# Kernel tuning notes

Hardware: AMD Instinct MI355X
Metric: run time of the kernel (lower is better)

## Reference

```python
import jax, jax.numpy as jnp
import numpy as np

FEATS = 768
HEAD = 12


def _phi(t):
    # elu feature map + 1 (guarantees positivity)
    return jax.nn.elu(t) + 1.0


def setup_inputs() -> dict:
    key = jax.random.key(0)
    ks = jax.random.split(key, 9)
    f = FEATS
    s = 1.0 / np.sqrt(f)
    x = jax.random.normal(ks[0], (4, 4096, f), dtype=jnp.float32)
    # weights stored as [in, out] so projection is x @ W + b
    Wq = jax.random.normal(ks[1], (f, f), dtype=jnp.float32) * s
    bq = jax.random.normal(ks[2], (f,), dtype=jnp.float32) * 0.01
    Wk = jax.random.normal(ks[3], (f, f), dtype=jnp.float32) * s
    bk = jax.random.normal(ks[4], (f,), dtype=jnp.float32) * 0.01
    Wv = jax.random.normal(ks[5], (f, f), dtype=jnp.float32) * s
    bv = jax.random.normal(ks[6], (f,), dtype=jnp.float32) * 0.01
    Wo = jax.random.normal(ks[7], (f, f), dtype=jnp.float32) * s
    bo = jax.random.normal(ks[8], (f,), dtype=jnp.float32) * 0.01
    return {"x": x, "Wq": Wq, "bq": bq, "Wk": Wk, "bk": bk,
            "Wv": Wv, "bv": bv, "Wo": Wo, "bo": bo}


def reference(x, Wq, bq, Wk, bk, Wv, bv, Wo, bo):
    b, n, f = x.shape
    h = HEAD
    d = f // h
    # project and split heads: [b, h, n, d]
    def heads(t):
        return t.reshape(b, n, h, d).transpose(0, 2, 1, 3)
    q = _phi(heads(x @ Wq + bq))
    k = _phi(heads(x @ Wk + bk))
    v = heads(x @ Wv + bv)
    # kv summary: [b, h, d, d] (sum over sequence)
    kv = jnp.einsum('bhnd,bhne->bhde', k, v)
    # normalizer: z[b,h,l] = 1 / (q[b,h,l,:] . sum_n k[b,h,n,:])  (no eps, as in source)
    ksum = k.sum(axis=2)                      # [b, h, d]
    z = 1.0 / jnp.einsum('bhld,bhd->bhl', q, ksum)  # [b, h, n]
    num = jnp.einsum('bhld,bhde->bhle', q, kv)      # [b, h, n, d]
    normed = num * z[..., None]                     # [b, h, n, d]
    out = normed.transpose(0, 2, 1, 3).reshape(b, n, f)  # [b, n, f]
    return out @ Wo + bo  # dropout p=0.0 -> identity
```

## Files before the change

### kernel.cpp

```cpp
#include <hip/hip_runtime.h>
#include <cstdint>
#include <cstddef>

#define DEVI __device__ __forceinline__

typedef short    shortx8 __attribute__((ext_vector_type(8)));
typedef short    shortx4 __attribute__((ext_vector_type(4)));
typedef short    shortx2 __attribute__((ext_vector_type(2)));
typedef __bf16   bf16x8  __attribute__((ext_vector_type(8)));
typedef float    floatx4 __attribute__((ext_vector_type(4)));

DEVI unsigned short f2b(float f) {
    union { float f; unsigned u; } a; a.f = f;
    unsigned r = a.u + 0x7fffu + ((a.u >> 16) & 1u);
    return (unsigned short)(r >> 16);
}
DEVI float b2f(unsigned short u) {
    union { unsigned u; float f; } a; a.u = ((unsigned)u) << 16;
    return a.f;
}

DEVI floatx4 mfma_bf16(bf16x8 a, bf16x8 b, floatx4 c) {
    return __builtin_amdgcn_mfma_f32_16x16x32_bf16(a, b, c, 0, 0, 0);
}

DEVI void glds16(const ushort* g, ushort* l) {
    __builtin_amdgcn_global_load_lds(
        (const __attribute__((address_space(1))) void*)g,
        (__attribute__((address_space(3))) void*)l, 16, 0, 0);
}

__global__ void k_prep(const float* __restrict__ x, ushort* __restrict__ xb,
                       const float* __restrict__ Wq, const float* __restrict__ Wk,
                       const float* __restrict__ Wv, const float* __restrict__ Wo,
                       ushort* __restrict__ Wt, ushort* __restrict__ Wot,
                       const float* __restrict__ bq, const float* __restrict__ bk,
                       const float* __restrict__ bv, float* __restrict__ bqkv) {
    __shared__ float tile[64][65];
    const int bid = blockIdx.x, t = threadIdx.x;
    if (bid < 6144) {
        size_t i = ((size_t)bid * 256 + t) * 8;
        float4 v0 = *(const float4*)(x + i);
        float4 v1 = *(const float4*)(x + i + 4);
        shortx8 o;
        o[0] = (short)f2b(v0.x); o[1] = (short)f2b(v0.y);
        o[2] = (short)f2b(v0.z); o[3] = (short)f2b(v0.w);
        o[4] = (short)f2b(v1.x); o[5] = (short)f2b(v1.y);
        o[6] = (short)f2b(v1.z); o[7] = (short)f2b(v1.w);
        *(shortx8*)(xb + i) = o;
    } else if (bid < 6720) {
        int pid = bid - 6144;
        int zi = pid / 144, rem = pid % 144;
        const float* W = (zi == 0) ? Wq : (zi == 1) ? Wk : (zi == 2) ? Wv : Wo;
        const int i0 = (rem / 12) * 64, j0 = (rem % 12) * 64;
        const int c = t & 63, r4 = t >> 6;
        for (int rr = r4; rr < 64; rr += 4)
            tile[rr][c] = W[(size_t)(i0 + rr) * 768 + j0 + c];
        __syncthreads();
        ushort* dst = (zi < 3) ? (Wt + (size_t)(zi * 768) * 768) : Wot;
        for (int jj = r4; jj < 64; jj += 4)
            dst[(size_t)(j0 + jj) * 768 + i0 + c] = f2b(tile[c][jj]);
    } else {
        int j = (bid - 6720) * 256 + t;
        if (j < 2304) {
            const float* src = (j < 768) ? bq : (j < 1536) ? bk : bv;
            bqkv[j] = src[j % 768];
        }
    }
}

template <int MODE>
__global__ __launch_bounds__(256, 4) void k_gemm(
    const ushort* __restrict__ A, const ushort* __restrict__ Bt,
    const float* __restrict__ bias, void* __restrict__ Cout, int Ncols) {
    constexpr int K = 768;
    constexpr int GY = (MODE == 0) ? 18 : 6;
    constexpr int NWG = 128 * GY;
    __shared__ ushort As[128 * 64];
    __shared__ ushort Bs[128 * 64];

    const int lin  = blockIdx.y * 128 + blockIdx.x;
    const int wg   = (lin & 7) * (NWG / 8) + (lin >> 3);
    const int band = wg / (8 * GY);
    const int rem  = wg % (8 * GY);
    const int m0 = (band * 8 + (rem & 7)) * 128;
    const int n0 = (rem >> 3) * 128;

    const int tid = threadIdx.x;
    const int w = tid >> 6, lane = tid & 63;

    const int lr = lane >> 3;
    const int lc = ((lane & 7) ^ lr) * 8;
    const ushort* aBase = A  + (size_t)(m0 + w * 32 + lr) * K + lc;
    const ushort* bBase = Bt + (size_t)(n0 + w * 32 + lr) * K + lc;
    ushort* aL = As + (w * 32) * 64;
    ushort* bL = Bs + (w * 32) * 64;

    const int rBase = (w >> 1) * 64;
    const int nBase = (w & 1) * 64;
    const int fr = lane & 15;
    const int q4 = lane >> 4;

    floatx4 acc[4][4] = {};

    for (int k0 = 0; k0 < K; k0 += 64) {
#pragma unroll
        for (int i = 0; i < 4; ++i) glds16(aBase + i * (8 * K) + k0, aL + i * (8 * 64));
#pragma unroll
        for (int i = 0; i < 4; ++i) glds16(bBase + i * (8 * K) + k0, bL + i * (8 * 64));
        __syncthreads();
#pragma unroll
        for (int kc = 0; kc < 2; ++kc) {
            const int off = ((kc * 4 + q4) ^ (fr & 7)) * 8;
            bf16x8 af[4], bf[4];
#pragma unroll
            for (int rt = 0; rt < 4; ++rt)
                af[rt] = *(const bf16x8*)(As + (rBase + rt * 16 + fr) * 64 + off);
#pragma unroll
            for (int nt = 0; nt < 4; ++nt)
                bf[nt] = *(const bf16x8*)(Bs + (nBase + nt * 16 + fr) * 64 + off);
#pragma unroll
            for (int rt = 0; rt < 4; ++rt)
#pragma unroll
                for (int nt = 0; nt < 4; ++nt)
                    acc[rt][nt] = mfma_bf16(af[rt], bf[nt], acc[rt][nt]);
        }
        __syncthreads();
    }

#pragma unroll
    for (int rt = 0; rt < 4; ++rt) {
#pragma unroll
        for (int nt = 0; nt < 4; ++nt) {
#pragma unroll
            for (int r = 0; r < 4; ++r) {
                int m = m0 + rBase + rt * 16 + q4 * 4 + r;
                int n = n0 + nBase + nt * 16 + fr;
                float v = acc[rt][nt][r] + bias[n];
                if (MODE == 0) {
                    if (n < 1536) v = (v > 0.f) ? (v + 1.f) : __expf(v);
                    ((ushort*)Cout)[(size_t)m * Ncols + n] = f2b(v);
                } else {
                    ((float*)Cout)[(size_t)m * Ncols + n] = v;
                }
            }
        }
    }
}

__global__ __launch_bounds__(256) void k_kv(const ushort* __restrict__ QKV,
                                            float* __restrict__ kvp) {
    const int bh = blockIdx.x, s = blockIdx.y;
    const int bb = bh / 12, head = bh % 12;
    __shared__ ushort kS[64 * 70];
    __shared__ ushort vS[64 * 70];
    const int t = threadIdx.x, w = t >> 6, lane = t & 63;
    const int fr = lane & 15, fk = (lane >> 4) * 8;

    floatx4 acc[5] = {};
    const int n_ld = t >> 2, c16 = (t & 3) * 16;
    const ushort* base = QKV + (size_t)(bb * 4096 + s * 512) * 2304 + 768 + head * 64 + c16;

    for (int rr = 0; rr < 8; ++rr) {
        if (rr) __syncthreads();
        {
            const ushort* kp = base + (size_t)(rr * 64 + n_ld) * 2304;
            union { shortx8 v8; shortx2 v2[4]; } k0, k1, v0, v1;
            k0.v8 = *(const shortx8*)(kp);
            k1.v8 = *(const shortx8*)(kp + 8);
            v0.v8 = *(const shortx8*)(kp + 768);
            v1.v8 = *(const shortx8*)(kp + 776);
            ushort* kd = kS + n_ld * 70 + c16;
            ushort* vd = vS + n_ld * 70 + c16;
#pragma unroll
            for (int i = 0; i < 4; ++i) {
                *(shortx2*)(kd + 2 * i)     = k0.v2[i];
                *(shortx2*)(kd + 8 + 2 * i) = k1.v2[i];
                *(shortx2*)(vd + 2 * i)     = v0.v2[i];
                *(shortx2*)(vd + 8 + 2 * i) = v1.v2[i];
            }
        }
        __syncthreads();
#pragma unroll
        for (int kl = 0; kl < 64; kl += 32) {
            union { bf16x8 v; ushort u[8]; } bfr, afr[4];
#pragma unroll
            for (int i = 0; i < 8; ++i) {
                int n = kl + fk + i;
                bfr.u[i] = kS[n * 70 + w * 16 + fr];
#pragma unroll
                for (int mt = 0; mt < 4; ++mt)
                    afr[mt].u[i] = vS[n * 70 + mt * 16 + fr];
            }
            union { bf16x8 v; ushort u[8]; } ones;
            ushort ov = (fr == 0) ? (ushort)0x3F80 : (ushort)0;
#pragma unroll
            for (int i = 0; i < 8; ++i) ones.u[i] = ov;
#pragma unroll
            for (int mt = 0; mt < 4; ++mt)
                acc[mt] = mfma_bf16(afr[mt].v, bfr.v, acc[mt]);
            acc[4] = mfma_bf16(ones.v, bfr.v, acc[4]);
        }
    }

    float* dst = kvp + ((size_t)bh * 8 + s) * (65 * 64);
#pragma unroll
    for (int mt = 0; mt < 4; ++mt)
#pragma unroll
        for (int r = 0; r < 4; ++r)
            dst[(mt * 16 + (lane >> 4) * 4 + r) * 64 + w * 16 + fr] = acc[mt][r];
    if (lane < 16) dst[64 * 64 + w * 16 + lane] = acc[4][0];
}

__global__ void k_kvred(const float* __restrict__ kvp, ushort* __restrict__ kvb) {
    int t4 = (blockIdx.x * 256 + threadIdx.x) * 4;
    int bh = t4 / 4160, rem = t4 % 4160;
    const float* p = kvp + (size_t)bh * 8 * 4160 + rem;
    float4 sum = {0.f, 0.f, 0.f, 0.f};
    for (int i = 0; i < 8; ++i) {
        float4 a = *(const float4*)(p + (size_t)i * 4160);
        sum.x += a.x; sum.y += a.y; sum.z += a.z; sum.w += a.w;
    }
    shortx4 o;
    o[0] = (short)f2b(sum.x); o[1] = (short)f2b(sum.y);
    o[2] = (short)f2b(sum.z); o[3] = (short)f2b(sum.w);
    *(shortx4*)(kvb + t4) = o;
}

__global__ __launch_bounds__(256) void k_num(const ushort* __restrict__ QKV,
                                             const ushort* __restrict__ kvb,
                                             ushort* __restrict__ normed) {
    const int bh = blockIdx.x, l0 = blockIdx.y * 128;
    const int bb = bh / 12, head = bh % 12;
    __shared__ ushort qsh[128 * 72];
    __shared__ ushort kvT[80 * 72];
    __shared__ float dnm[128];
    const int t = threadIdx.x, w = t >> 6, lane = t & 63;

    {
        const ushort* kvbb = kvb + (size_t)bh * 4160;
        int c8 = (t & 7) * 8;
        for (int r0 = (t >> 3); r0 < 65; r0 += 32)
            *(shortx8*)(kvT + r0 * 72 + c8) = *(const shortx8*)(kvbb + r0 * 64 + c8);
    }
    for (int idx = t; idx < 15 * 72; idx += 256) kvT[65 * 72 + idx] = 0;

    const ushort* qg = QKV + (size_t)(bb * 4096 + l0) * 2304 + head * 64;
    {
        int row = t >> 3, c8 = (t & 7) * 8;
#pragma unroll
        for (int i = 0; i < 4; ++i) {
            shortx8 v = *(const shortx8*)(qg + (size_t)(i * 32 + row) * 2304 + c8);
            *(shortx8*)(qsh + (i * 32 + row) * 72 + c8) = v;
        }
    }
    __syncthreads();

    const int fr = lane & 15, fk = (lane >> 4) * 8;
    floatx4 acc[2][5] = {};
#pragma unroll
    for (int kc = 0; kc < 2; ++kc) {
        bf16x8 a[2], b[5];
#pragma unroll
        for (int rt = 0; rt < 2; ++rt)
            a[rt] = *(const bf16x8*)(qsh + (w * 32 + rt * 16 + fr) * 72 + kc * 32 + fk);
#pragma unroll
        for (int nt = 0; nt < 5; ++nt)
            b[nt] = *(const bf16x8*)(kvT + (nt * 16 + fr) * 72 + kc * 32 + fk);
#pragma unroll
        for (int rt = 0; rt < 2; ++rt)
#pragma unroll
            for (int nt = 0; nt < 5; ++nt)
                acc[rt][nt] = mfma_bf16(a[rt], b[nt], acc[rt][nt]);
    }
    if (fr == 0) {
#pragma unroll
        for (int rt = 0; rt < 2; ++rt)
#pragma unroll
            for (int r = 0; r < 4; ++r)
                dnm[w * 32 + rt * 16 + (lane >> 4) * 4 + r] = acc[rt][4][r];
    }
    __syncthreads();
#pragma unroll
    for (int rt = 0; rt < 2; ++rt) {
#pragma unroll
        for (int r = 0; r < 4; ++r) {
            int ml = w * 32 + rt * 16 + (lane >> 4) * 4 + r;
            float z = 1.f / dnm[ml];
            size_t base = (size_t)(bb * 4096 + l0 + ml) * 768 + head * 64;
#pragma unroll
            for (int nt = 0; nt < 4; ++nt)
                normed[base + nt * 16 + fr] = f2b(acc[rt][nt][r] * z);
        }
    }
}

extern "C" void kernel_launch(void* const* d_in, const int* in_sizes, int n_in,
                              void* d_out, int out_size, void* d_ws, size_t ws_size,
                              hipStream_t stream) {
    const float* x  = (const float*)d_in[0];
    const float* Wq = (const float*)d_in[1];
    const float* bq = (const float*)d_in[2];
    const float* Wk = (const float*)d_in[3];
    const float* bk = (const float*)d_in[4];
    const float* Wv = (const float*)d_in[5];
    const float* bv = (const float*)d_in[6];
    const float* Wo = (const float*)d_in[7];
    const float* bo = (const float*)d_in[8];

    char* ws = (char*)d_ws;
    ushort* Xb   = (ushort*)(ws);
    ushort* Wt   = (ushort*)(ws + 25165824);
    ushort* Wot  = (ushort*)(ws + 28704768);
    float*  bqkv = (float*)(ws + 29884416);
    ushort* QKV  = (ushort*)(ws + 29893632);
    float*  kvp  = (float*)(ws + 105391104);
    ushort* kvb  = (ushort*)(ws + 111780864);
    ushort* normed = Xb;

    k_prep <<<dim3(6729),      256, 0, stream>>>(x, Xb, Wq, Wk, Wv, Wo, Wt, Wot,
                                                 bq, bk, bv, bqkv);
    k_gemm<0><<<dim3(128, 18), 256, 0, stream>>>(Xb, Wt, bqkv, (void*)QKV, 2304);
    k_kv   <<<dim3(48, 8),     256, 0, stream>>>(QKV, kvp);
    k_kvred<<<dim3(195),       256, 0, stream>>>(kvp, kvb);
    k_num  <<<dim3(48, 32),    256, 0, stream>>>(QKV, kvb, normed);
    k_gemm<1><<<dim3(128, 6),  256, 0, stream>>>(normed, Wot, bo, d_out, 768);
}
```

Baseline: 229.7 us.

## Replace KV partial-sum reduction kernel with atomics and double-buffer KV loads

The separate k_kvred reduction kernel is removed. k_kv now accumulates its partial kv summaries straight into a float buffer with atomicAdd, and that buffer is zeroed by extra blocks in k_prep. k_kv splits the sequence into 16 chunks instead of 8 to give more blocks, and double-buffers its shared-memory tiles so global loads overlap the MFMA work. k_num reads the float kv and converts it to bf16 itself. This saves a launch and a round trip through memory, at the cost of atomic contention and a float summation order that is no longer deterministic.

```diff
diff --git a/kernel.cpp b/kernel.cpp
--- a/kernel.cpp
+++ b/kernel.cpp
@@ -35,7 +35,8 @@
                        const float* __restrict__ Wv, const float* __restrict__ Wo,
                        ushort* __restrict__ Wt, ushort* __restrict__ Wot,
                        const float* __restrict__ bq, const float* __restrict__ bk,
-                       const float* __restrict__ bv, float* __restrict__ bqkv) {
+                       const float* __restrict__ bv, float* __restrict__ bqkv,
+                       float* __restrict__ kvp) {
     __shared__ float tile[64][65];
     const int bid = blockIdx.x, t = threadIdx.x;
     if (bid < 6144) {
@@ -60,12 +61,16 @@
         ushort* dst = (zi < 3) ? (Wt + (size_t)(zi * 768) * 768) : Wot;
         for (int jj = r4; jj < 64; jj += 4)
             dst[(size_t)(j0 + jj) * 768 + i0 + c] = f2b(tile[c][jj]);
-    } else {
+    } else if (bid < 6729) {
         int j = (bid - 6720) * 256 + t;
         if (j < 2304) {
             const float* src = (j < 768) ? bq : (j < 1536) ? bk : bv;
             bqkv[j] = src[j % 768];
         }
+    } else {
+        int idx = (bid - 6729) * 1024 + t * 4;
+        float4 z = {0.f, 0.f, 0.f, 0.f};
+        *(float4*)(kvp + idx) = z;
     }
 }
 
@@ -148,87 +153,89 @@
     }
 }
 
+#define KV_LOAD(rr, r)  do {                                          \
+    const ushort* kp = base + (size_t)((rr) * 64 + n_ld) * 2304;      \
+    r[0] = *(const shortx8*)(kp);                                     \
+    r[1] = *(const shortx8*)(kp + 8);                                 \
+    r[2] = *(const shortx8*)(kp + 768);                               \
+    r[3] = *(const shortx8*)(kp + 776); } while (0)
+
+#define KV_STORE(buf, r) do {                                         \
+    union { shortx8 v8; shortx2 v2[4]; } u0, u1, u2, u3;              \
+    u0.v8 = r[0]; u1.v8 = r[1]; u2.v8 = r[2]; u3.v8 = r[3];           \
+    ushort* kd = kS[buf] + n_ld * 70 + c16;                           \
+    ushort* vd = vS[buf] + n_ld * 70 + c16;                           \
+    _Pragma("unroll")                                                 \
+    for (int i = 0; i < 4; ++i) {                                     \
+        *(shortx2*)(kd + 2 * i)     = u0.v2[i];                       \
+        *(shortx2*)(kd + 8 + 2 * i) = u1.v2[i];                       \
+        *(shortx2*)(vd + 2 * i)     = u2.v2[i];                       \
+        *(shortx2*)(vd + 8 + 2 * i) = u3.v2[i]; } } while (0)
+
 __global__ __launch_bounds__(256) void k_kv(const ushort* __restrict__ QKV,
                                             float* __restrict__ kvp) {
     const int bh = blockIdx.x, s = blockIdx.y;
     const int bb = bh / 12, head = bh % 12;
-    __shared__ ushort kS[64 * 70];
-    __shared__ ushort vS[64 * 70];
+    __shared__ ushort kS[2][64 * 70];
+    __shared__ ushort vS[2][64 * 70];
     const int t = threadIdx.x, w = t >> 6, lane = t & 63;
     const int fr = lane & 15, fk = (lane >> 4) * 8;
 
     floatx4 acc[5] = {};
     const int n_ld = t >> 2, c16 = (t & 3) * 16;
-    const ushort* base = QKV + (size_t)(bb * 4096 + s * 512) * 2304 + 768 + head * 64 + c16;
-
-    for (int rr = 0; rr < 8; ++rr) {
-        if (rr) __syncthreads();
-        {
-            const ushort* kp = base + (size_t)(rr * 64 + n_ld) * 2304;
-            union { shortx8 v8; shortx2 v2[4]; } k0, k1, v0, v1;
-            k0.v8 = *(const shortx8*)(kp);
-            k1.v8 = *(const shortx8*)(kp + 8);
-            v0.v8 = *(const shortx8*)(kp + 768);
-            v1.v8 = *(const shortx8*)(kp + 776);
-            ushort* kd = kS + n_ld * 70 + c16;
-            ushort* vd = vS + n_ld * 70 + c16;
-#pragma unroll
-            for (int i = 0; i < 4; ++i) {
-                *(shortx2*)(kd + 2 * i)     = k0.v2[i];
-                *(shortx2*)(kd + 8 + 2 * i) = k1.v2[i];
-                *(shortx2*)(vd + 2 * i)     = v0.v2[i];
-                *(shortx2*)(vd + 8 + 2 * i) = v1.v2[i];
-            }
-        }
+    const ushort* base = QKV + (size_t)(bb * 4096 + s * 256) * 2304 + 768 + head * 64 + c16;
+
+    union { bf16x8 v; ushort u[8]; } ones;
+    {
+        ushort ov = (fr == 0) ? (ushort)0x3F80 : (ushort)0;
+#pragma unroll
+        for (int i = 0; i < 8; ++i) ones.u[i] = ov;
+    }
+
+    shortx8 rA[4], rB[4];
+    KV_LOAD(0, rA);
+    KV_STORE(0, rA);
+
+#pragma unroll
+    for (int rr = 0; rr < 4; ++rr) {
         __syncthreads();
+        if (rr == 0)      KV_LOAD(1, rB);
+        else if (rr == 1) KV_LOAD(2, rA);
+        else if (rr == 2) KV_LOAD(3, rB);
+        const int buf = rr & 1;
 #pragma unroll
         for (int kl = 0; kl < 64; kl += 32) {
             union { bf16x8 v; ushort u[8]; } bfr, afr[4];
 #pragma unroll
             for (int i = 0; i < 8; ++i) {
                 int n = kl + fk + i;
-                bfr.u[i] = kS[n * 70 + w * 16 + fr];
+                bfr.u[i] = kS[buf][n * 70 + w * 16 + fr];
 #pragma unroll
                 for (int mt = 0; mt < 4; ++mt)
-                    afr[mt].u[i] = vS[n * 70 + mt * 16 + fr];
+                    afr[mt].u[i] = vS[buf][n * 70 + mt * 16 + fr];
             }
-            union { bf16x8 v; ushort u[8]; } ones;
-            ushort ov = (fr == 0) ? (ushort)0x3F80 : (ushort)0;
-#pragma unroll
-            for (int i = 0; i < 8; ++i) ones.u[i] = ov;
 #pragma unroll
             for (int mt = 0; mt < 4; ++mt)
                 acc[mt] = mfma_bf16(afr[mt].v, bfr.v, acc[mt]);
             acc[4] = mfma_bf16(ones.v, bfr.v, acc[4]);
         }
-    }
-
-    float* dst = kvp + ((size_t)bh * 8 + s) * (65 * 64);
+        if (rr == 0)      KV_STORE(1, rB);
+        else if (rr == 1) KV_STORE(0, rA);
+        else if (rr == 2) KV_STORE(1, rB);
+    }
+
+    float* dst = kvp + (size_t)bh * (65 * 64);
 #pragma unroll
     for (int mt = 0; mt < 4; ++mt)
 #pragma unroll
         for (int r = 0; r < 4; ++r)
-            dst[(mt * 16 + (lane >> 4) * 4 + r) * 64 + w * 16 + fr] = acc[mt][r];
-    if (lane < 16) dst[64 * 64 + w * 16 + lane] = acc[4][0];
-}
-
-__global__ void k_kvred(const float* __restrict__ kvp, ushort* __restrict__ kvb) {
-    int t4 = (blockIdx.x * 256 + threadIdx.x) * 4;
-    int bh = t4 / 4160, rem = t4 % 4160;
-    const float* p = kvp + (size_t)bh * 8 * 4160 + rem;
-    float4 sum = {0.f, 0.f, 0.f, 0.f};
-    for (int i = 0; i < 8; ++i) {
-        float4 a = *(const float4*)(p + (size_t)i * 4160);
-        sum.x += a.x; sum.y += a.y; sum.z += a.z; sum.w += a.w;
-    }
-    shortx4 o;
-    o[0] = (short)f2b(sum.x); o[1] = (short)f2b(sum.y);
-    o[2] = (short)f2b(sum.z); o[3] = (short)f2b(sum.w);
-    *(shortx4*)(kvb + t4) = o;
+            atomicAdd(dst + (mt * 16 + (lane >> 4) * 4 + r) * 64 + w * 16 + fr,
+                      acc[mt][r]);
+    if (lane < 16) atomicAdd(dst + 64 * 64 + w * 16 + lane, acc[4][0]);
 }
 
 __global__ __launch_bounds__(256) void k_num(const ushort* __restrict__ QKV,
-                                             const ushort* __restrict__ kvb,
+                                             const float* __restrict__ kvp,
                                              ushort* __restrict__ normed) {
     const int bh = blockIdx.x, l0 = blockIdx.y * 128;
     const int bb = bh / 12, head = bh % 12;
@@ -238,10 +245,15 @@
     const int t = threadIdx.x, w = t >> 6, lane = t & 63;
 
     {
-        const ushort* kvbb = kvb + (size_t)bh * 4160;
-        int c8 = (t & 7) * 8;
-        for (int r0 = (t >> 3); r0 < 65; r0 += 32)
-            *(shortx8*)(kvT + r0 * 72 + c8) = *(const shortx8*)(kvbb + r0 * 64 + c8);
+        const float* kvf = kvp + (size_t)bh * 4160;
+        int c4 = (t & 15) * 4;
+        for (int r0 = (t >> 4); r0 < 65; r0 += 16) {
+            float4 a = *(const float4*)(kvf + r0 * 64 + c4);
+            shortx4 o;
+            o[0] = (short)f2b(a.x); o[1] = (short)f2b(a.y);
+            o[2] = (short)f2b(a.z); o[3] = (short)f2b(a.w);
+            *(shortx4*)(kvT + r0 * 72 + c4) = o;
+        }
     }
     for (int idx = t; idx < 15 * 72; idx += 256) kvT[65 * 72 + idx] = 0;
 
@@ -315,14 +327,12 @@
     float*  bqkv = (float*)(ws + 29884416);
     ushort* QKV  = (ushort*)(ws + 29893632);
     float*  kvp  = (float*)(ws + 105391104);
-    ushort* kvb  = (ushort*)(ws + 111780864);
     ushort* normed = Xb;
 
-    k_prep <<<dim3(6729),      256, 0, stream>>>(x, Xb, Wq, Wk, Wv, Wo, Wt, Wot,
-                                                 bq, bk, bv, bqkv);
+    k_prep <<<dim3(6924),      256, 0, stream>>>(x, Xb, Wq, Wk, Wv, Wo, Wt, Wot,
+                                                 bq, bk, bv, bqkv, kvp);
     k_gemm<0><<<dim3(128, 18), 256, 0, stream>>>(Xb, Wt, bqkv, (void*)QKV, 2304);
-    k_kv   <<<dim3(48, 8),     256, 0, stream>>>(QKV, kvp);
-    k_kvred<<<dim3(195),       256, 0, stream>>>(kvp, kvb);
-    k_num  <<<dim3(48, 32),    256, 0, stream>>>(QKV, kvb, normed);
+    k_kv   <<<dim3(48, 16),    256, 0, stream>>>(QKV, kvp);
+    k_num  <<<dim3(48, 32),    256, 0, stream>>>(QKV, kvp, normed);
     k_gemm<1><<<dim3(128, 6),  256, 0, stream>>>(normed, Wot, bo, d_out, 768);
 }
```

New measurement: 236.6 us. 3.0% more time.
